# Optimization experiments

Hardware: AMD Instinct MI355X
Metric: run time of the kernel (lower is better)

Reference implementation:

```python
import jax, jax.numpy as jnp
import numpy as np
from jax import lax

EPS = 1e-5

# Straight-through identity binarization (torch code mutates .data, so autograd
# sees binarized values but grads flow as identity to the latent weights/inputs).
def ste_sign(x):
    return x + lax.stop_gradient(jnp.sign(x) - x)

# SignActivation: sign forward, hard-tanh-style gradient (zero where |i| > 1).
@jax.custom_vjp
def sign_act(x):
    return jnp.sign(x)

def _sa_fwd(x):
    return jnp.sign(x), x

def _sa_bwd(x, g):
    return (jnp.where(jnp.abs(x) <= 1.0, g, 0.0),)

sign_act.defvjp(_sa_fwd, _sa_bwd)

def bn2d(x, gamma, beta):
    # training-mode BatchNorm2d: batch stats over (N,H,W), biased variance
    mean = jnp.mean(x, axis=(0, 2, 3), keepdims=True)
    var = jnp.var(x, axis=(0, 2, 3), keepdims=True)
    xn = (x - mean) * lax.rsqrt(var + EPS)
    return xn * gamma.reshape(1, -1, 1, 1) + beta.reshape(1, -1, 1, 1)

def bn1d(x, gamma, beta):
    mean = jnp.mean(x, axis=0, keepdims=True)
    var = jnp.var(x, axis=0, keepdims=True)
    xn = (x - mean) * lax.rsqrt(var + EPS)
    return xn * gamma[None, :] + beta[None, :]

def conv2d(x, w, stride, pad):
    return lax.conv_general_dilated(
        x, w, window_strides=(stride, stride),
        padding=((pad, pad), (pad, pad)),
        dimension_numbers=("NCHW", "OIHW", "NCHW"))


def setup_inputs() -> dict:
    key = jax.random.key(0)
    ks = jax.random.split(key, 4)
    width = 0.01
    x = jax.random.normal(ks[0], (8192, 1, 28, 28), dtype=jnp.float32)
    w1 = jax.random.normal(ks[1], (32, 1, 5, 5), dtype=jnp.float32) * width
    w2 = jax.random.normal(ks[2], (64, 32, 4, 4), dtype=jnp.float32) * width
    w3 = jax.random.normal(ks[3], (10, 64 * 64), dtype=jnp.float32) * width
    g1 = jnp.ones((32,), jnp.float32); b1 = jnp.zeros((32,), jnp.float32)
    g2 = jnp.ones((64,), jnp.float32); b2 = jnp.zeros((64,), jnp.float32)
    g3 = jnp.ones((10,), jnp.float32); b3 = jnp.zeros((10,), jnp.float32)
    return {"x": x, "w1": w1, "g1": g1, "b1": b1,
            "w2": w2, "g2": g2, "b2": b2,
            "w3": w3, "g3": g3, "b3": b3}


def reference(x, w1, g1, b1, w2, g2, b2, w3, g3, b3):
    # cv1: input channels = 1 != 3 -> input binarized; weight binarized
    h = conv2d(ste_sign(x), ste_sign(w1), stride=2, pad=2)   # [B,32,14,14]
    h = bn2d(h, g1, b1)
    h = sign_act(h)
    # cv2: input channels 32 != 3 -> binarized (no-op on +-1 values)
    h = conv2d(ste_sign(h), ste_sign(w2), stride=2, pad=2)   # [B,64,8,8]
    h = bn2d(h, g2, b2)
    h = sign_act(h)
    h = h.reshape(h.shape[0], -1)                            # [B,4096]
    # fc3: features 4096 != 784 -> binarized (no-op on +-1 values)
    h = jnp.dot(ste_sign(h), ste_sign(w3).T)                 # [B,10]
    h = bn1d(h, g3, b3)
    return h
```

## Files before the change

### kernel.cpp

```cpp
#include <hip/hip_runtime.h>
#include <stdint.h>


#define NB 8192
typedef unsigned long long ull;

#define OFF_C1  ((size_t)0)
#define SZ_C1   ((size_t)NB*6272)
#define OFF_C2  (OFF_C1 + SZ_C1)
#define SZ_C2   ((size_t)NB*4096)
#define OFF_FC  (OFF_C2 + SZ_C2)
#define SZ_FC   ((size_t)NB*10*4)
#define OFF_S1  (OFF_FC + SZ_FC)
#define OFF_S2  (OFF_S1 + 2048)
#define OFF_S3  (OFF_S2 + 8192)
#define OFF_W2B (OFF_S3 + 2048)
#define OFF_W3B (OFF_W2B + 4096)

__device__ inline void mk_thresh(double s, double t, int &T, int &flip) {
    if (s > 0.0) {
        int v = (int)floor(-t / s) - 2;
        for (int c = 0; c < 6; ++c) { if (s * (double)v + t > 0.0) break; ++v; }
        T = v; flip = 0;
    } else if (s < 0.0) {
        int v = (int)floor(-t / s) - 2;
        for (int c = 0; c < 6; ++c) { if (!(s * (double)v + t > 0.0)) break; ++v; }
        T = v; flip = 1;
    } else { T = -200; flip = (t > 0.0) ? 0 : 1; }
}
__device__ inline int clampT(int T, int lim) {
    return (T < -lim) ? -lim : (T > lim) ? lim : T;
}

__global__ __launch_bounds__(256) void kA_conv1(
    const float* __restrict__ x, const float* __restrict__ w1,
    const float* __restrict__ w2, const float* __restrict__ w3,
    int8_t* __restrict__ c1out, int* __restrict__ stats1,
    ull* __restrict__ w2bT, ull* __restrict__ w3b)
{
    const int tid = threadIdx.x, lane = tid & 63, wv = tid >> 6;

    if (blockIdx.x >= 2048) {
        const int t = (blockIdx.x - 2048)*256 + tid;
        if (t < 512) {
            const int idx = t >> 6, k = t & 63;
            const int u = idx >> 1, pr = idx & 1;
            uint32_t lo = 0u, hi = 0u;
            #pragma unroll 8
            for (int c = 0; c < 32; ++c) {
                const float* wp = w2 + (((k*32 + c)*4 + u)*4 + 2*pr);
                lo |= (wp[0] > 0.f ? 1u : 0u) << c;
                hi |= (wp[1] > 0.f ? 1u : 0u) << c;
            }
            w2bT[t] = (ull)lo | ((ull)hi << 32);
        } else if (t < 1152) {
            const int w = t - 512;
            const float* wp = w3 + (size_t)(w >> 6)*4096 + (size_t)(w & 63)*64;
            ull bits = 0ull;
            #pragma unroll 16
            for (int k = 0; k < 64; ++k)
                bits |= (ull)(wp[k] > 0.f ? 1 : 0) << k;
            w3b[w] = bits;
        }
        return;
    }

    __shared__ ull sxb[4][16];
    __shared__ uint32_t wfilt[32];
    __shared__ uint32_t outb[4][1568];
    __shared__ int lsum[32], lsq[32];

    if (tid < 32) {
        uint32_t f = 0u;
        #pragma unroll
        for (int q = 0; q < 25; ++q) f |= (w1[tid*25 + q] > 0.f ? 1u : 0u) << q;
        wfilt[tid] = f;
        lsum[tid] = 0; lsq[tid] = 0;
    }
    __syncthreads();
    const int n = blockIdx.x*4 + wv;
    #pragma unroll
    for (int t = 0; t < 13; ++t) {
        const int idx = t*64 + lane;
        const float v = (idx < 784) ? x[(size_t)n*784 + idx] : -1.f;
        const ull bal = __ballot(v > 0.f);
        if (lane == t) sxb[wv][t] = bal;
    }
    if (lane == 13) sxb[wv][13] = 0ull;
    for (int t = 0; t < 4; ++t) {
        const int p = t*64 + lane;
        if (p < 196) {
            const int i = p / 14, j = p - i*14;
            const uint32_t cmask = (j == 0) ? 0x1Cu : (j == 13) ? 0x0Fu : 0x1Fu;
            uint32_t win = 0u, vm = 0u;
            #pragma unroll
            for (int u = 0; u < 5; ++u) {
                const int r = 2*i + u - 2;
                if (r >= 0 && r < 28) {
                    const int bp = 28*r, w0 = bp >> 6, sh = bp & 63;
                    const ull a = sxb[wv][w0], b = sxb[wv][w0+1];
                    uint32_t row = (uint32_t)((a >> sh) | ((b << 1) << (63 - sh)));
                    row = (row & 0x0FFFFFFFu) << 2;
                    win |= ((row >> (2*j)) & 31u) << (5*u);
                    vm  |= cmask << (5*u);
                }
            }
            const int nv = __popc(vm);
            uint32_t dw[8];
            #pragma unroll
            for (int d = 0; d < 8; ++d) dw[d] = 0u;
            #pragma unroll
            for (int c = 0; c < 32; ++c) {
                const int diff = __popc((win ^ wfilt[c]) & vm);
                const int o = nv - 2*diff;
                dw[c >> 2] |= (uint32_t)(o & 255) << (8*(c & 3));
            }
            #pragma unroll
            for (int d = 0; d < 8; ++d) outb[wv][p*8 + d] = dw[d];
        }
    }
    {
        int4* dst = (int4*)(c1out + (size_t)n*6272);
        const int4* src = (const int4*)&outb[wv][0];
        #pragma unroll
        for (int t = 0; t < 7; ++t) {
            const int idx = t*64 + lane;
            if (idx < 392) dst[idx] = src[idx];
        }
    }
    {
        int s4[4] = {0,0,0,0}, q4[4] = {0,0,0,0};
        const uint32_t* ob32 = &outb[wv][0];
        #pragma unroll
        for (int t = 0; t < 25; ++t) {
            const int idx = t*64 + lane;
            if (idx < 1568) {
                const uint32_t dwv = ob32[idx];
                #pragma unroll
                for (int qq = 0; qq < 4; ++qq) {
                    const int v = (int)((int8_t)(dwv >> (8*qq)));
                    s4[qq] += v; q4[qq] += v*v;
                }
            }
        }
        #pragma unroll
        for (int off = 8; off <= 32; off <<= 1) {
            #pragma unroll
            for (int qq = 0; qq < 4; ++qq) {
                s4[qq] += __shfl_xor(s4[qq], off);
                q4[qq] += __shfl_xor(q4[qq], off);
            }
        }
        if (lane < 8) {
            #pragma unroll
            for (int qq = 0; qq < 4; ++qq) {
                atomicAdd(&lsum[lane*4 + qq], s4[qq]);
                atomicAdd(&lsq[lane*4 + qq], q4[qq]);
            }
        }
    }
    __syncthreads();
    if (tid < 32) {
        const int shard = blockIdx.x & 7;
        atomicAdd(&stats1[(shard*32 + tid)*2 + 0], lsum[tid]);
        atomicAdd(&stats1[(shard*32 + tid)*2 + 1], lsq[tid]);
    }
}

__global__ __launch_bounds__(256) void kB_conv2(
    const int8_t* __restrict__ c1out, const int* __restrict__ stats1,
    const float* __restrict__ gm1, const float* __restrict__ bt1,
    const ull* __restrict__ w2bT,
    int8_t* __restrict__ c2out, ull* __restrict__ stats2)
{
    __shared__ uint32_t BwU[4][14][16];
    __shared__ int sT1[4][32];
    __shared__ uint32_t cw[4][64][17];
    __shared__ int ssum[64], ssq[64];
    const int tid = threadIdx.x, lane = tid & 63, wv = tid >> 6;
    const int n = blockIdx.x*4 + wv;

    uint32_t Wlo[8], Whi[8];
    #pragma unroll
    for (int idx = 0; idx < 8; ++idx) {
        const uint2 w = ((const uint2*)w2bT)[idx*64 + lane];
        Wlo[idx] = w.x; Whi[idx] = w.y;
    }

    if (tid < 64) { ssum[tid] = 0; ssq[tid] = 0; }
    int fl = 0;
    if (lane < 32) {
        long long s = 0, q = 0;
        for (int sh = 0; sh < 8; ++sh) {
            s += stats1[(sh*32 + lane)*2 + 0];
            q += stats1[(sh*32 + lane)*2 + 1];
        }
        const double N = 8192.0 * 196.0;
        const double mean = (double)s / N;
        const double var  = (double)q / N - mean*mean;
        const double a = (double)gm1[lane] / sqrt(var + 1e-5);
        const double b = (double)bt1[lane] - mean*a;
        int T; mk_thresh(a, b, T, fl);
        sT1[wv][lane] = clampT(T, 26);
    }
    const uint32_t flipn1 = ~(uint32_t)__ballot(fl != 0);
    __syncthreads();

    for (int t = lane; t < 196; t += 64) {
        const int r = t / 14, c = t - r*14;
        const uint4* src = (const uint4*)(c1out + ((size_t)n*196 + t)*32);
        const uint4 lo4 = src[0], hi4 = src[1];
        const uint32_t wsrc[8] = {lo4.x, lo4.y, lo4.z, lo4.w, hi4.x, hi4.y, hi4.z, hi4.w};
        uint32_t neg = 0u;
        #pragma unroll
        for (int d = 0; d < 8; ++d) {
            #pragma unroll
            for (int qq = 0; qq < 4; ++qq) {
                const int ch = d*4 + qq;
                const int v = (int)((int8_t)(wsrc[d] >> (8*qq)));
                neg |= ((uint32_t)(v - sT1[wv][ch]) >> 31) << ch;
            }
        }
        BwU[wv][r][c] = neg ^ flipn1;
    }

    uint32_t PA[32], PB[32];
#define LOADP(BUF, K)                                                          \
    {                                                                          \
        const uint4* r0 = (const uint4*)&BwU[wv][2*(K)][0];                    \
        const uint4* r1 = (const uint4*)&BwU[wv][2*(K)+1][0];                  \
        _Pragma("unroll")                                                      \
        for (int tt = 0; tt < 4; ++tt) {                                       \
            const uint4 v0 = r0[tt];                                           \
            BUF[4*tt+0] = v0.x; BUF[4*tt+1] = v0.y;                            \
            BUF[4*tt+2] = v0.z; BUF[4*tt+3] = v0.w;                            \
            const uint4 v1 = r1[tt];                                           \
            BUF[16+4*tt+0] = v1.x; BUF[16+4*tt+1] = v1.y;                      \
            BUF[16+4*tt+2] = v1.z; BUF[16+4*tt+3] = v1.w;                      \
        }                                                                      \
    }
#define UT(BUF, RO, UU)                                                        \
    {                                                                          \
        if (j >= 1) { D += __popc(BUF[(RO)*16 + 2*j-2] ^ Wlo[2*(UU)])          \
                         + __popc(BUF[(RO)*16 + 2*j-1] ^ Whi[2*(UU)]);   ++nw; } \
        if (j <= 6) { D += __popc(BUF[(RO)*16 + 2*j]   ^ Wlo[2*(UU)+1])        \
                         + __popc(BUF[(RO)*16 + 2*j+1] ^ Whi[2*(UU)+1]); ++nw; } \
    }
    int s = 0, q = 0;
    LOADP(PA, 0)
    #pragma unroll
    for (int i = 0; i < 8; ++i) {
        if (i >= 1 && i <= 6) {
            if (i & 1) { LOADP(PB, i) } else { LOADP(PA, i) }
        }
        uint32_t o0 = 0u, o1 = 0u;
        #pragma unroll
        for (int j = 0; j < 8; ++j) {
            int D = 0, nw = 0;
            if (i >= 1) {
                if ((i-1) & 1) { UT(PB, 0, 0) UT(PB, 1, 1) }
                else           { UT(PA, 0, 0) UT(PA, 1, 1) }
            }
            if (i <= 6) {
                if (i & 1) { UT(PB, 0, 2) UT(PB, 1, 3) }
                else       { UT(PA, 0, 2) UT(PA, 1, 3) }
            }
            const int o = 32*nw - D;
            s += o; q += o*o;
            if (j < 4) o0 |= (uint32_t)(o & 255) << (8*j);
            else       o1 |= (uint32_t)(o & 255) << (8*(j-4));
        }
        cw[wv][lane][2*i]     = o0;
        cw[wv][lane][2*i + 1] = o1;
    }
#undef LOADP
#undef UT
    atomicAdd(&ssum[lane], s);
    atomicAdd(&ssq[lane], q);
    {
        uint32_t* dst = (uint32_t*)(c2out + (size_t)n*4096);
        #pragma unroll
        for (int t = 0; t < 16; ++t) {
            const int g = t*64 + lane;
            dst[g] = cw[wv][g >> 4][g & 15];
        }
    }
    __syncthreads();
    if (tid < 64) {
        const int shard = blockIdx.x & 7;
        atomicAdd(&stats2[(shard*64 + tid)*2 + 0], (ull)(long long)ssum[tid]);
        atomicAdd(&stats2[(shard*64 + tid)*2 + 1], (ull)(long long)ssq[tid]);
    }
}

__global__ __launch_bounds__(256) void kC_fc(
    const int8_t* __restrict__ c2o, const float* __restrict__ gm2,
    const float* __restrict__ bt2, const ull* __restrict__ stats2,
    const ull* __restrict__ w3b,
    int* __restrict__ fc, ull* __restrict__ stats3)
{
    __shared__ int fco[4][10];
    __shared__ int s3[10], q3[10];
    const int tid = threadIdx.x, lane = tid & 63, wv = tid >> 6;
    if (tid < 10) { s3[tid] = 0; q3[tid] = 0; }
    int T2, fl;
    {
        long long ss = 0, qq = 0;
        for (int sh = 0; sh < 8; ++sh) {
            ss += (long long)stats2[(sh*64 + lane)*2 + 0];
            qq += (long long)stats2[(sh*64 + lane)*2 + 1];
        }
        const double N = 8192.0 * 64.0;
        const double mh = (double)ss / N;
        const double vh = (double)qq / N - mh*mh;
        const double a = (double)gm2[lane] / sqrt(4.0*vh + 1e-5);
        const double b = (double)bt2[lane] - 2.0*mh*a;
        int T; mk_thresh(2.0*a, b, T, fl);
        T2 = clampT(T, 200);
    }
    const ull flipn2 = ~__ballot(fl != 0);
    const int n = blockIdx.x*4 + wv;
    const uint4* src = (const uint4*)(c2o + (size_t)n*4096 + lane*64);
    uint32_t neglo = 0u, neghi = 0u;
    #pragma unroll
    for (int r4 = 0; r4 < 4; ++r4) {
        const uint4 v4 = src[r4];
        const uint32_t wsrc[4] = {v4.x, v4.y, v4.z, v4.w};
        #pragma unroll
        for (int cc = 0; cc < 4; ++cc) {
            #pragma unroll
            for (int b = 0; b < 4; ++b) {
                const int p = r4*16 + cc*4 + b;
                const int v = (int)((int8_t)(wsrc[cc] >> (8*b)));
                const uint32_t bit = (uint32_t)(v - T2) >> 31;
                if (p < 32) neglo |= bit << p; else neghi |= bit << (p - 32);
            }
        }
    }
    const ull myw = ((ull)neglo | ((ull)neghi << 32)) ^ flipn2;
    uint32_t pk[5];
    #pragma unroll
    for (int t = 0; t < 5; ++t) {
        const uint32_t pa = (uint32_t)__popcll(myw ^ w3b[(2*t+0)*64 + lane]);
        const uint32_t pb = (uint32_t)__popcll(myw ^ w3b[(2*t+1)*64 + lane]);
        pk[t] = pa | (pb << 16);
    }
    #pragma unroll
    for (int off = 32; off >= 1; off >>= 1) {
        #pragma unroll
        for (int t = 0; t < 5; ++t) pk[t] += __shfl_xor(pk[t], off);
    }
    if (lane == 0) {
        #pragma unroll
        for (int m = 0; m < 10; ++m) {
            const int tot = (pk[m >> 1] >> (16*(m & 1))) & 0xFFFF;
            fco[wv][m] = 4096 - 2*tot;
        }
    }
    __syncthreads();
    if (tid < 40) {
        const int li = tid / 10, m = tid - li*10;
        const int o = fco[li][m];
        fc[(size_t)(blockIdx.x*4 + li)*10 + m] = o;
        atomicAdd(&s3[m], o);
        atomicAdd(&q3[m], o*o);
    }
    __syncthreads();
    if (tid < 10) {
        const int shard = blockIdx.x & 7;
        atomicAdd(&stats3[(shard*10 + tid)*2 + 0], (ull)(long long)s3[tid]);
        atomicAdd(&stats3[(shard*10 + tid)*2 + 1], (ull)(long long)q3[tid]);
    }
}

__global__ __launch_bounds__(256) void kD_apply(
    const int* __restrict__ fc, const float* __restrict__ gm3,
    const float* __restrict__ bt3, const ull* __restrict__ stats3,
    float* __restrict__ out)
{
    __shared__ float a3[10], b3[10];
    const int tid = threadIdx.x;
    if (tid < 10) {
        long long s = 0, q = 0;
        for (int sh = 0; sh < 8; ++sh) {
            s += (long long)stats3[(sh*10 + tid)*2 + 0];
            q += (long long)stats3[(sh*10 + tid)*2 + 1];
        }
        const double N = 8192.0;
        const double mean = (double)s / N;
        const double var  = (double)q / N - mean*mean;
        const double a = (double)gm3[tid] / sqrt(var + 1e-5);
        a3[tid] = (float)a;
        b3[tid] = (float)((double)bt3[tid] - mean*a);
    }
    __syncthreads();
    const int e = blockIdx.x*256 + tid;
    if (e < NB*10) {
        const int m = e % 10;
        out[e] = fmaf(a3[m], (float)fc[e], b3[m]);
    }
}

extern "C" void kernel_launch(void* const* d_in, const int* in_sizes, int n_in,
                              void* d_out, int out_size, void* d_ws, size_t ws_size,
                              hipStream_t stream)
{
    const float* x   = (const float*)d_in[0];
    const float* w1  = (const float*)d_in[1];
    const float* gm1 = (const float*)d_in[2];
    const float* bt1 = (const float*)d_in[3];
    const float* w2  = (const float*)d_in[4];
    const float* gm2 = (const float*)d_in[5];
    const float* bt2 = (const float*)d_in[6];
    const float* w3  = (const float*)d_in[7];
    const float* gm3 = (const float*)d_in[8];
    const float* bt3 = (const float*)d_in[9];
    char* ws = (char*)d_ws;
    int8_t* c1o = (int8_t*)(ws + OFF_C1);
    int8_t* c2o = (int8_t*)(ws + OFF_C2);
    int*    fcb = (int*)(ws + OFF_FC);
    int*    s1  = (int*)(ws + OFF_S1);
    ull*    s2  = (ull*)(ws + OFF_S2);
    ull*    s3  = (ull*)(ws + OFF_S3);
    ull*    w2bp = (ull*)(ws + OFF_W2B);
    ull*    w3bp = (ull*)(ws + OFF_W3B);

    (void)hipMemsetAsync(ws + OFF_S1, 0, 12288, stream);
    kA_conv1<<<2053, 256, 0, stream>>>(x, w1, w2, w3, c1o, s1, w2bp, w3bp);
    kB_conv2<<<2048, 256, 0, stream>>>(c1o, s1, gm1, bt1, w2bp, c2o, s2);
    kC_fc   <<<2048, 256, 0, stream>>>(c2o, gm2, bt2, s2, w3bp, fcb, s3);
    kD_apply<<<320,  256, 0, stream>>>(fcb, gm3, bt3, s3, (float*)d_out);
}
```

Baseline: 181.6 us.

## Finalize BN thresholds in last-arriving block and store conv2 output directly

Each stage kernel now counts finished blocks with an atomic counter, and the last block to arrive turns the sharded statistics into BN thresholds (or scale/shift) once, writing them to workspace. The next kernel no longer repeats the per-block double-precision reduction and threshold search, it just loads the precomputed values. Separately, conv2 writes its int8 output straight to global memory as uint4 stores instead of staging it through a large shared-memory transpose buffer, which cuts LDS use and may raise occupancy. The cost is one extra fence and atomic per block, plus correctness that depends on the counter reset, since the counters sit inside the region that is memset each launch.

```diff
diff --git a/kernel.cpp b/kernel.cpp
--- a/kernel.cpp
+++ b/kernel.cpp
@@ -14,6 +14,10 @@
 #define OFF_S1  (OFF_FC + SZ_FC)
 #define OFF_S2  (OFF_S1 + 2048)
 #define OFF_S3  (OFF_S2 + 8192)
+#define OFF_CNT (OFF_S3 + 1280)
+#define OFF_T1  (OFF_S3 + 1344)
+#define OFF_T2  (OFF_S3 + 1504)
+#define OFF_AB3 (OFF_S3 + 1792)
 #define OFF_W2B (OFF_S3 + 2048)
 #define OFF_W3B (OFF_W2B + 4096)
 
@@ -35,8 +39,10 @@
 __global__ __launch_bounds__(256) void kA_conv1(
     const float* __restrict__ x, const float* __restrict__ w1,
     const float* __restrict__ w2, const float* __restrict__ w3,
+    const float* __restrict__ gm1, const float* __restrict__ bt1,
     int8_t* __restrict__ c1out, int* __restrict__ stats1,
-    ull* __restrict__ w2bT, ull* __restrict__ w3b)
+    ull* __restrict__ w2bT, ull* __restrict__ w3b,
+    int* __restrict__ T1g, int* __restrict__ cntA)
 {
     const int tid = threadIdx.x, lane = tid & 63, wv = tid >> 6;
 
@@ -69,6 +75,7 @@
     __shared__ uint32_t wfilt[32];
     __shared__ uint32_t outb[4][1568];
     __shared__ int lsum[32], lsq[32];
+    __shared__ int lastA;
 
     if (tid < 32) {
         uint32_t f = 0u;
@@ -165,18 +172,41 @@
         atomicAdd(&stats1[(shard*32 + tid)*2 + 0], lsum[tid]);
         atomicAdd(&stats1[(shard*32 + tid)*2 + 1], lsq[tid]);
     }
+    __syncthreads();
+    if (tid == 0) {
+        __threadfence();
+        lastA = (atomicAdd(cntA, 1) == 2047) ? 1 : 0;
+    }
+    __syncthreads();
+    if (lastA && tid < 32) {
+        long long s = 0, q = 0;
+        for (int sh = 0; sh < 8; ++sh) {
+            s += atomicAdd(&stats1[(sh*32 + tid)*2 + 0], 0);
+            q += atomicAdd(&stats1[(sh*32 + tid)*2 + 1], 0);
+        }
+        const double N = 8192.0 * 196.0;
+        const double mean = (double)s / N;
+        const double var  = (double)q / N - mean*mean;
+        const double a = (double)gm1[tid] / sqrt(var + 1e-5);
+        const double b = (double)bt1[tid] - mean*a;
+        int T, fl; mk_thresh(a, b, T, fl);
+        T1g[tid] = clampT(T, 26);
+        const uint32_t fn1 = ~(uint32_t)__ballot(fl != 0);
+        if (tid == 0) T1g[32] = (int)fn1;
+    }
 }
 
 __global__ __launch_bounds__(256) void kB_conv2(
-    const int8_t* __restrict__ c1out, const int* __restrict__ stats1,
-    const float* __restrict__ gm1, const float* __restrict__ bt1,
-    const ull* __restrict__ w2bT,
-    int8_t* __restrict__ c2out, ull* __restrict__ stats2)
+    const int8_t* __restrict__ c1out, const int* __restrict__ T1g,
+    const ull* __restrict__ w2bT, const float* __restrict__ gm2,
+    const float* __restrict__ bt2,
+    int8_t* __restrict__ c2out, ull* __restrict__ stats2,
+    int* __restrict__ T2g, int* __restrict__ cntB)
 {
     __shared__ uint32_t BwU[4][14][16];
-    __shared__ int sT1[4][32];
-    __shared__ uint32_t cw[4][64][17];
+    __shared__ int sT1[32];
     __shared__ int ssum[64], ssq[64];
+    __shared__ int lastB;
     const int tid = threadIdx.x, lane = tid & 63, wv = tid >> 6;
     const int n = blockIdx.x*4 + wv;
 
@@ -188,22 +218,8 @@
     }
 
     if (tid < 64) { ssum[tid] = 0; ssq[tid] = 0; }
-    int fl = 0;
-    if (lane < 32) {
-        long long s = 0, q = 0;
-        for (int sh = 0; sh < 8; ++sh) {
-            s += stats1[(sh*32 + lane)*2 + 0];
-            q += stats1[(sh*32 + lane)*2 + 1];
-        }
-        const double N = 8192.0 * 196.0;
-        const double mean = (double)s / N;
-        const double var  = (double)q / N - mean*mean;
-        const double a = (double)gm1[lane] / sqrt(var + 1e-5);
-        const double b = (double)bt1[lane] - mean*a;
-        int T; mk_thresh(a, b, T, fl);
-        sT1[wv][lane] = clampT(T, 26);
-    }
-    const uint32_t flipn1 = ~(uint32_t)__ballot(fl != 0);
+    if (tid < 32) sT1[tid] = T1g[tid];
+    const uint32_t flipn1 = (uint32_t)T1g[32];
     __syncthreads();
 
     for (int t = lane; t < 196; t += 64) {
@@ -218,7 +234,7 @@
             for (int qq = 0; qq < 4; ++qq) {
                 const int ch = d*4 + qq;
                 const int v = (int)((int8_t)(wsrc[d] >> (8*qq)));
-                neg |= ((uint32_t)(v - sT1[wv][ch]) >> 31) << ch;
+                neg |= ((uint32_t)(v - sT1[ch]) >> 31) << ch;
             }
         }
         BwU[wv][r][c] = neg ^ flipn1;
@@ -247,6 +263,8 @@
                          + __popc(BUF[(RO)*16 + 2*j+1] ^ Whi[2*(UU)+1]); ++nw; } \
     }
     int s = 0, q = 0;
+    uint32_t* dst32 = (uint32_t*)(c2out + (size_t)n*4096 + (size_t)lane*64);
+    uint32_t p0 = 0u, p1 = 0u;
     LOADP(PA, 0)
     #pragma unroll
     for (int i = 0; i < 8; ++i) {
@@ -270,55 +288,57 @@
             if (j < 4) o0 |= (uint32_t)(o & 255) << (8*j);
             else       o1 |= (uint32_t)(o & 255) << (8*(j-4));
         }
-        cw[wv][lane][2*i]     = o0;
-        cw[wv][lane][2*i + 1] = o1;
+        if ((i & 1) == 0) { p0 = o0; p1 = o1; }
+        else *(uint4*)(dst32 + 4*(i >> 1)) = make_uint4(p0, p1, o0, o1);
     }
 #undef LOADP
 #undef UT
     atomicAdd(&ssum[lane], s);
     atomicAdd(&ssq[lane], q);
-    {
-        uint32_t* dst = (uint32_t*)(c2out + (size_t)n*4096);
-        #pragma unroll
-        for (int t = 0; t < 16; ++t) {
-            const int g = t*64 + lane;
-            dst[g] = cw[wv][g >> 4][g & 15];
-        }
-    }
     __syncthreads();
     if (tid < 64) {
         const int shard = blockIdx.x & 7;
         atomicAdd(&stats2[(shard*64 + tid)*2 + 0], (ull)(long long)ssum[tid]);
         atomicAdd(&stats2[(shard*64 + tid)*2 + 1], (ull)(long long)ssq[tid]);
     }
+    __syncthreads();
+    if (tid == 0) {
+        __threadfence();
+        lastB = (atomicAdd(cntB, 1) == 2047) ? 1 : 0;
+    }
+    __syncthreads();
+    if (lastB && tid < 64) {
+        long long ss = 0, qq = 0;
+        for (int sh = 0; sh < 8; ++sh) {
+            ss += (long long)atomicAdd(&stats2[(sh*64 + tid)*2 + 0], 0ull);
+            qq += (long long)atomicAdd(&stats2[(sh*64 + tid)*2 + 1], 0ull);
+        }
+        const double N = 8192.0 * 64.0;
+        const double mh = (double)ss / N;
+        const double vh = (double)qq / N - mh*mh;
+        const double a = (double)gm2[tid] / sqrt(4.0*vh + 1e-5);
+        const double b = (double)bt2[tid] - 2.0*mh*a;
+        int T, fl; mk_thresh(2.0*a, b, T, fl);
+        T2g[tid] = clampT(T, 200);
+        const ull fn2 = ~__ballot(fl != 0);
+        if (tid == 0) *(ull*)(T2g + 64) = fn2;
+    }
 }
 
 __global__ __launch_bounds__(256) void kC_fc(
-    const int8_t* __restrict__ c2o, const float* __restrict__ gm2,
-    const float* __restrict__ bt2, const ull* __restrict__ stats2,
-    const ull* __restrict__ w3b,
-    int* __restrict__ fc, ull* __restrict__ stats3)
+    const int8_t* __restrict__ c2o, const int* __restrict__ T2g,
+    const ull* __restrict__ w3b, const float* __restrict__ gm3,
+    const float* __restrict__ bt3,
+    int* __restrict__ fc, ull* __restrict__ stats3,
+    float* __restrict__ ab3, int* __restrict__ cntC)
 {
     __shared__ int fco[4][10];
     __shared__ int s3[10], q3[10];
+    __shared__ int lastC;
     const int tid = threadIdx.x, lane = tid & 63, wv = tid >> 6;
     if (tid < 10) { s3[tid] = 0; q3[tid] = 0; }
-    int T2, fl;
-    {
-        long long ss = 0, qq = 0;
-        for (int sh = 0; sh < 8; ++sh) {
-            ss += (long long)stats2[(sh*64 + lane)*2 + 0];
-            qq += (long long)stats2[(sh*64 + lane)*2 + 1];
-        }
-        const double N = 8192.0 * 64.0;
-        const double mh = (double)ss / N;
-        const double vh = (double)qq / N - mh*mh;
-        const double a = (double)gm2[lane] / sqrt(4.0*vh + 1e-5);
-        const double b = (double)bt2[lane] - 2.0*mh*a;
-        int T; mk_thresh(2.0*a, b, T, fl);
-        T2 = clampT(T, 200);
-    }
-    const ull flipn2 = ~__ballot(fl != 0);
+    const int T2 = T2g[lane];
+    const ull flipn2 = *(const ull*)(T2g + 64);
     const int n = blockIdx.x*4 + wv;
     const uint4* src = (const uint4*)(c2o + (size_t)n*4096 + lane*64);
     uint32_t neglo = 0u, neghi = 0u;
@@ -371,28 +391,34 @@
         atomicAdd(&stats3[(shard*10 + tid)*2 + 0], (ull)(long long)s3[tid]);
         atomicAdd(&stats3[(shard*10 + tid)*2 + 1], (ull)(long long)q3[tid]);
     }
+    __syncthreads();
+    if (tid == 0) {
+        __threadfence();
+        lastC = (atomicAdd(cntC, 1) == 2047) ? 1 : 0;
+    }
+    __syncthreads();
+    if (lastC && tid < 10) {
+        long long s = 0, q = 0;
+        for (int sh = 0; sh < 8; ++sh) {
+            s += (long long)atomicAdd(&stats3[(sh*10 + tid)*2 + 0], 0ull);
+            q += (long long)atomicAdd(&stats3[(sh*10 + tid)*2 + 1], 0ull);
+        }
+        const double N = 8192.0;
+        const double mean = (double)s / N;
+        const double var  = (double)q / N - mean*mean;
+        const double a = (double)gm3[tid] / sqrt(var + 1e-5);
+        ab3[tid] = (float)a;
+        ab3[10 + tid] = (float)((double)bt3[tid] - mean*a);
+    }
 }
 
 __global__ __launch_bounds__(256) void kD_apply(
-    const int* __restrict__ fc, const float* __restrict__ gm3,
-    const float* __restrict__ bt3, const ull* __restrict__ stats3,
+    const int* __restrict__ fc, const float* __restrict__ ab3,
     float* __restrict__ out)
 {
     __shared__ float a3[10], b3[10];
     const int tid = threadIdx.x;
-    if (tid < 10) {
-        long long s = 0, q = 0;
-        for (int sh = 0; sh < 8; ++sh) {
-            s += (long long)stats3[(sh*10 + tid)*2 + 0];
-            q += (long long)stats3[(sh*10 + tid)*2 + 1];
-        }
-        const double N = 8192.0;
-        const double mean = (double)s / N;
-        const double var  = (double)q / N - mean*mean;
-        const double a = (double)gm3[tid] / sqrt(var + 1e-5);
-        a3[tid] = (float)a;
-        b3[tid] = (float)((double)bt3[tid] - mean*a);
-    }
+    if (tid < 10) { a3[tid] = ab3[tid]; b3[tid] = ab3[10 + tid]; }
     __syncthreads();
     const int e = blockIdx.x*256 + tid;
     if (e < NB*10) {
@@ -422,12 +448,19 @@
     int*    s1  = (int*)(ws + OFF_S1);
     ull*    s2  = (ull*)(ws + OFF_S2);
     ull*    s3  = (ull*)(ws + OFF_S3);
+    int*    cnt = (int*)(ws + OFF_CNT);
+    int*    T1g = (int*)(ws + OFF_T1);
+    int*    T2g = (int*)(ws + OFF_T2);
+    float*  ab3 = (float*)(ws + OFF_AB3);
     ull*    w2bp = (ull*)(ws + OFF_W2B);
     ull*    w3bp = (ull*)(ws + OFF_W3B);
 
     (void)hipMemsetAsync(ws + OFF_S1, 0, 12288, stream);
-    kA_conv1<<<2053, 256, 0, stream>>>(x, w1, w2, w3, c1o, s1, w2bp, w3bp);
-    kB_conv2<<<2048, 256, 0, stream>>>(c1o, s1, gm1, bt1, w2bp, c2o, s2);
-    kC_fc   <<<2048, 256, 0, stream>>>(c2o, gm2, bt2, s2, w3bp, fcb, s3);
-    kD_apply<<<320,  256, 0, stream>>>(fcb, gm3, bt3, s3, (float*)d_out);
-}
+    kA_conv1<<<2053, 256, 0, stream>>>(x, w1, w2, w3, gm1, bt1, c1o, s1,
+                                       w2bp, w3bp, T1g, cnt + 0);
+    kB_conv2<<<2048, 256, 0, stream>>>(c1o, T1g, w2bp, gm2, bt2, c2o, s2,
+                                       T2g, cnt + 1);
+    kC_fc   <<<2048, 256, 0, stream>>>(c2o, T2g, w3bp, gm3, bt3, fcb, s3,
+                                       ab3, cnt + 2);
+    kD_apply<<<320,  256, 0, stream>>>(fcb, ab3, (float*)d_out);
+}
```

New measurement: 378.4 us. 108% more time.
